# Optimization experiments

Hardware: AMD Instinct MI355X
Metric: run time of the kernel (lower is better)

Reference implementation:

```python
import jax, jax.numpy as jnp
import numpy as np
from jax import lax

INPUT_DIM = 1024
HIDDEN_DIM = 2048
N, L = 64, 512


def setup_inputs() -> dict:
    key = jax.random.key(0)
    ks = jax.random.split(key, 6)
    X = jax.random.normal(ks[0], (N, L, INPUT_DIM), dtype=jnp.float32)
    H0 = jnp.zeros((N, HIDDEN_DIM), dtype=jnp.float32)
    # G-invariant layer params (DeepSets invariant map): out = w * sum(x) + b, one per gate (i,f,g,o)
    inv_scale = 1.0 / np.sqrt(INPUT_DIM)
    inv_w = jax.random.normal(ks[1], (4, HIDDEN_DIM), dtype=jnp.float32) * inv_scale
    inv_b = jax.random.normal(ks[2], (4, HIDDEN_DIM), dtype=jnp.float32) * inv_scale
    # Linear(hidden, hidden) per gate, torch convention W: (out, in)
    lin_scale = 1.0 / np.sqrt(HIDDEN_DIM)
    lin_W = jax.random.normal(ks[3], (4, HIDDEN_DIM, HIDDEN_DIM), dtype=jnp.float32) * lin_scale
    lin_b = jax.random.normal(ks[4], (4, HIDDEN_DIM), dtype=jnp.float32) * lin_scale
    return {"X": X, "H0": H0, "inv_w": inv_w, "inv_b": inv_b, "lin_W": lin_W, "lin_b": lin_b}


def reference(X, H0, inv_w, inv_b, lin_W, lin_b):
    # X: (N, L, D); H0: (N, H)
    def step(carry, x_t):
        h, c = carry                               # (N, H), (N, H)
        s = jnp.sum(x_t, axis=-1, keepdims=True)   # (N, 1) invariant statistic
        inv = s * inv_w[:, None, :] + inv_b[:, None, :]            # (4, N, H)
        lin = jnp.einsum('nh,gkh->gnk', h, lin_W) + lin_b[:, None, :]  # (4, N, H)
        z = inv + lin
        i = jax.nn.sigmoid(z[0])
        f = jax.nn.sigmoid(z[1])
        g = jnp.tanh(z[2])
        o = jax.nn.sigmoid(z[3])
        c = f * c + i * g
        h = o * jnp.tanh(c)
        return (h, c), None

    Xt = jnp.swapaxes(X, 0, 1)                     # (L, N, D)
    (h, _), _ = lax.scan(step, (H0, jnp.zeros_like(H0)), Xt)
    # original returns swapdims(hidden_state, 0, 1) -> (H, N)
    return h.T
```

## Files before the change

kernel.cpp:

```cpp
#include <hip/hip_runtime.h>
#include <hip/hip_fp16.h>


typedef _Float16 f16x8 __attribute__((ext_vector_type(8)));
typedef float    f32x4 __attribute__((ext_vector_type(4)));
typedef unsigned long long u64;

static __device__ __forceinline__ float fast_sig(float x) {
  return 1.f / (1.f + __expf(-x));
}
static __device__ __forceinline__ float fast_tanh(float x) {
  x = fminf(15.f, fmaxf(-15.f, x));
  const float e = __expf(2.f * x);
  return (e - 1.f) / (e + 1.f);
}

static __device__ __forceinline__ void st_h16(void* p, float v) {
  const unsigned short b = __builtin_bit_cast(unsigned short, (_Float16)v);
  __hip_atomic_store((unsigned short*)p, b, __ATOMIC_RELAXED, __HIP_MEMORY_SCOPE_AGENT);
}
static __device__ __forceinline__ void st_h32(void* p, unsigned v) {
  __hip_atomic_store((unsigned*)p, v, __ATOMIC_RELAXED, __HIP_MEMORY_SCOPE_AGENT);
}

static __device__ __forceinline__ int h_off(int n, int j) {
  return ((n >> 4) << 16) + ((j >> 5) << 10) + ((n & 15) << 6) +
         (((j >> 3) & 3) << 4) + ((j & 7) << 1);
}

__global__ void __launch_bounds__(256) seq_sum_kernel(const float* __restrict__ X,
                                                      float* s_all) {
  const int gw   = (int)((blockIdx.x * blockDim.x + threadIdx.x) >> 6);
  const int lane = threadIdx.x & 63;
  const int n = gw >> 9, t = gw & 511;
  const float4* p = (const float4*)(X + ((size_t)gw << 10));
  float s = 0.f;
#pragma unroll
  for (int i = 0; i < 4; ++i) {
    const float4 v = p[lane + (i << 6)];
    s += (v.x + v.y) + (v.z + v.w);
  }
#pragma unroll
  for (int off = 32; off; off >>= 1) s += __shfl_xor(s, off);
  if (lane == 0) s_all[(t << 6) + n] = s;
}

__global__ void bar_init_kernel(unsigned* bar) {
  bar[threadIdx.x]       = 0u;
  bar[threadIdx.x + 256] = 0u;
  bar[threadIdx.x + 512] = 0u;
  bar[threadIdx.x + 768] = 0u;
}

static __device__ __forceinline__ void grid_barrier(unsigned* bar, unsigned round,
                                                    int tid, int blk) {
  asm volatile("s_waitcnt vmcnt(0)" ::: "memory");
  __syncthreads();
  if (tid == 0) {
    __hip_atomic_fetch_add(bar + ((blk & 7) << 4), 1u, __ATOMIC_RELAXED,
                           __HIP_MEMORY_SCOPE_AGENT);
    const unsigned target = round << 8;
    unsigned guard = 0;
    for (;;) {
      unsigned s = 0;
#pragma unroll
      for (int i = 0; i < 8; ++i)
        s += __hip_atomic_load(bar + (i << 4), __ATOMIC_RELAXED,
                               __HIP_MEMORY_SCOPE_AGENT);
      if (s >= target) break;
      __builtin_amdgcn_s_sleep(1);
      if (++guard > (1u << 23)) break;
    }
  }
  __syncthreads();
}

#define LOAD4(d0, d1, d2, d3, addr)                                         \
  asm volatile("global_load_dwordx4 %0, %4, off sc1\n\t"                    \
               "global_load_dwordx4 %1, %4, off offset:1024 sc1\n\t"        \
               "global_load_dwordx4 %2, %4, off offset:2048 sc1\n\t"        \
               "global_load_dwordx4 %3, %4, off offset:3072 sc1"            \
               : "=&v"(d0), "=&v"(d1), "=&v"(d2), "=&v"(d3)                 \
               : "v"(addr)                                                  \
               : "memory")

#define WAITG(n, A)                                                         \
  asm volatile("s_waitcnt vmcnt(" #n ")"                                    \
               : "+v"(A[0]), "+v"(A[1]), "+v"(A[2]), "+v"(A[3]),            \
                 "+v"(A[4]), "+v"(A[5]), "+v"(A[6]), "+v"(A[7]),            \
                 "+v"(A[8]), "+v"(A[9]), "+v"(A[10]), "+v"(A[11]),          \
                 "+v"(A[12]), "+v"(A[13]), "+v"(A[14]), "+v"(A[15])         \
               :                                                            \
               : "memory")

#define KMATH(A)                                                            \
  _Pragma("unroll")                                                         \
  for (int i_ = 0; i_ < 16; ++i_) {                                         \
    acc[0] = __builtin_amdgcn_mfma_f32_16x16x32_f16(A[i_], Wr[i_][0],       \
                                                    acc[0], 0, 0, 0);       \
    acc[1] = __builtin_amdgcn_mfma_f32_16x16x32_f16(A[i_], Wr[i_][1],       \
                                                    acc[1], 0, 0, 0);       \
    acc[2] = __builtin_amdgcn_mfma_f32_16x16x32_f16(A[i_], Wr[i_][2],       \
                                                    acc[2], 0, 0, 0);       \
    acc[3] = __builtin_amdgcn_mfma_f32_16x16x32_f16(A[i_], Wr[i_][3],       \
                                                    acc[3], 0, 0, 0);       \
  }

#define SCATTER(bt)                                                         \
  _Pragma("unroll")                                                         \
  for (int ct_ = 0; ct_ < 4; ++ct_) {                                       \
    const int kf_ = ct_ * 4 + (cc >> 2);                                    \
    _Pragma("unroll")                                                       \
    for (int v_ = 0; v_ < 4; ++v_) {                                        \
      const int n_  = (bt) * 16 + (q << 2) + v_;                            \
      const int key = (n_ & 15) ^ (n_ >> 4);                                \
      red[wave][n_][((kf_ ^ key) << 2) + (cc & 3)] = acc[ct_][v_];          \
    }                                                                       \
  }

__global__ void __launch_bounds__(256, 1) ginv_lstm_persist(
    const float* __restrict__ lin_W, const float* __restrict__ inv_w,
    const float* __restrict__ inv_b, const float* __restrict__ lin_b,
    const float* s_all, const float* __restrict__ H0,
    _Float16* hb0, _Float16* hb1, unsigned* bar, float* out) {
  __shared__ __align__(16) float s_lds[512][32];
  __shared__ __align__(16) float red[4][32][64];
  const int blk = blockIdx.x;
  const int tid = threadIdx.x;
  _Float16* hbuf[2] = {hb0, hb1};

  const int fblk = blk & 127;
  const int nh   = blk >> 7;

  const int wave = tid >> 6;
  const int lane = tid & 63;
  const int q    = lane >> 4;
  const int cc   = lane & 15;

  f16x8 Wr[16][4];
#pragma unroll
  for (int ct = 0; ct < 4; ++ct) {
    const int kf = ct * 4 + (cc >> 2), g = cc & 3;
    const float* wrow =
        lin_W + (((size_t)(g * 2048 + fblk * 16 + kf)) << 11) + wave * 512 + q * 8;
#pragma unroll
    for (int kc = 0; kc < 16; ++kc) {
      const float4 va = *(const float4*)(wrow + kc * 32);
      const float4 vb = *(const float4*)(wrow + kc * 32 + 4);
      f16x8 f;
      f[0] = (_Float16)va.x; f[1] = (_Float16)va.y;
      f[2] = (_Float16)va.z; f[3] = (_Float16)va.w;
      f[4] = (_Float16)vb.x; f[5] = (_Float16)vb.y;
      f[6] = (_Float16)vb.z; f[7] = (_Float16)vb.w;
      Wr[kc][ct] = f;
    }
  }

  {
    int i0 = blk * 512 + tid;
    st_h16((char*)hb0 + h_off(i0 >> 11, i0 & 2047), H0[i0]);
    i0 += 256;
    st_h16((char*)hb0 + h_off(i0 >> 11, i0 & 2047), H0[i0]);
  }

  for (int i = tid; i < 512 * 8; i += 256) {
    const int t4 = i >> 3, nl4 = (i & 7) << 2;
    *(float4*)&s_lds[t4][nl4] =
        *(const float4*)&s_all[(t4 << 6) + (nh << 5) + nl4];
  }

  const int nloc = (wave << 3) + (lane >> 3);
  const int c0   = (lane & 7) << 1;
  float iw[2][4], ibb[2][4];
#pragma unroll
  for (int kk = 0; kk < 2; ++kk) {
    const int Kg = fblk * 16 + c0 + kk;
#pragma unroll
    for (int g = 0; g < 4; ++g) {
      iw[kk][g]  = inv_w[(g << 11) + Kg];
      ibb[kk][g] = inv_b[(g << 11) + Kg] + lin_b[(g << 11) + Kg];
    }
  }

  unsigned round = 1;
  grid_barrier(bar, round, tid, blk);

  float cst[2] = {0.f, 0.f};
  float hnew[2] = {0.f, 0.f};

  const int ld_base = ((nh * 2) << 16) + (wave << 14) + (cc << 6) + (q << 4);
  const int hst_off = ((nh * 2 + (nloc >> 4)) << 16) + ((fblk >> 1) << 10) +
                      ((nloc & 15) << 6) + ((fblk & 1) << 5) + (c0 << 1);
  const int key = (nloc & 15) ^ (nloc >> 4);

  for (int t = 0; t < 512; ++t) {
    const char* hpb = (const char*)hbuf[t & 1] + ld_base;

    f16x8 pa[16], pb[16];
    f32x4 acc[4];

#pragma unroll
    for (int w = 0; w < 4; ++w)
      LOAD4(pa[w * 4], pa[w * 4 + 1], pa[w * 4 + 2], pa[w * 4 + 3],
            hpb + (w << 12));
#pragma unroll
    for (int w = 0; w < 4; ++w)
      LOAD4(pb[w * 4], pb[w * 4 + 1], pb[w * 4 + 2], pb[w * 4 + 3],
            hpb + 65536 + (w << 12));

    WAITG(16, pa);
#pragma unroll
    for (int ct = 0; ct < 4; ++ct) acc[ct] = (f32x4){0.f, 0.f, 0.f, 0.f};
    KMATH(pa);
    SCATTER(0);

    WAITG(0, pb);
#pragma unroll
    for (int ct = 0; ct < 4; ++ct) acc[ct] = (f32x4){0.f, 0.f, 0.f, 0.f};
    KMATH(pb);
    SCATTER(1);

    __syncthreads();

    const float sv = s_lds[t][nloc];
#pragma unroll
    for (int kk = 0; kk < 2; ++kk) {
      const int off = ((c0 + kk) ^ key) << 2;
      f32x4 zz = *(const f32x4*)&red[0][nloc][off];
#pragma unroll
      for (int w = 1; w < 4; ++w) zz += *(const f32x4*)&red[w][nloc][off];
      const float zi = zz[0] + sv * iw[kk][0] + ibb[kk][0];
      const float zf = zz[1] + sv * iw[kk][1] + ibb[kk][1];
      const float zg = zz[2] + sv * iw[kk][2] + ibb[kk][2];
      const float zo = zz[3] + sv * iw[kk][3] + ibb[kk][3];
      const float ig = fast_sig(zi);
      const float fg = fast_sig(zf);
      const float gg = fast_tanh(zg);
      const float og = fast_sig(zo);
      const float cn = fg * cst[kk] + ig * gg;
      cst[kk] = cn;
      hnew[kk] = og * fast_tanh(cn);
    }

    {
      const unsigned lo = __builtin_bit_cast(unsigned short, (_Float16)hnew[0]);
      const unsigned hi = __builtin_bit_cast(unsigned short, (_Float16)hnew[1]);
      st_h32((char*)hbuf[(t + 1) & 1] + hst_off, lo | (hi << 16));
    }
    ++round;
    grid_barrier(bar, round, tid, blk);
  }

#pragma unroll
  for (int kk = 0; kk < 2; ++kk)
    out[((fblk * 16 + c0 + kk) << 6) + (nh << 5) + nloc] = hnew[kk];
}

extern "C" void kernel_launch(void* const* d_in, const int* in_sizes, int n_in,
                              void* d_out, int out_size, void* d_ws, size_t ws_size,
                              hipStream_t stream) {
  const float* X     = (const float*)d_in[0];
  const float* H0    = (const float*)d_in[1];
  const float* inv_w = (const float*)d_in[2];
  const float* inv_b = (const float*)d_in[3];
  const float* lin_W = (const float*)d_in[4];
  const float* lin_b = (const float*)d_in[5];
  float* out = (float*)d_out;

  const size_t S_BYTES = 512 * 64 * 4;
  const size_t BAR_PAD = 4096;
  const size_t H_BYTES = 64 * 2048 * 2;
  const size_t NEED = S_BYTES + BAR_PAD + 2 * H_BYTES;

  float*    s_all;
  unsigned* bar;
  _Float16* hb[2];
  if (ws_size >= NEED) {
    char* ws = (char*)d_ws;
    s_all = (float*)ws;
    bar   = (unsigned*)(ws + S_BYTES);
    for (int i = 0; i < 2; ++i)
      hb[i] = (_Float16*)(ws + S_BYTES + BAR_PAD + (size_t)i * H_BYTES);
  } else {
    s_all = (float*)d_out;
    char* xt = (char*)d_in[0] + (size_t)64 * 512 * 1024 * 4 -
               (BAR_PAD + 2 * H_BYTES);
    bar = (unsigned*)xt;
    for (int i = 0; i < 2; ++i)
      hb[i] = (_Float16*)(xt + BAR_PAD + (size_t)i * H_BYTES);
  }

  seq_sum_kernel<<<8192, 256, 0, stream>>>(X, s_all);
  bar_init_kernel<<<1, 256, 0, stream>>>(bar);
  ginv_lstm_persist<<<256, 256, 0, stream>>>(lin_W, inv_w, inv_b, lin_b, s_all, H0,
                                             hb[0], hb[1], bar, out);
}
```

Baseline: 4.194 ms.

## Use two-level tree grid barrier and staggered per-chunk load waits

Replaces the flat grid barrier, where each waiting block polled eight counters, with a hierarchy. Blocks increment a group counter, the last arrival in each group bumps a root counter, and waiters spin on that single root word. Separately, the single wait on all sixteen loads of each half is split into four waits on four-load chunks, so MFMA work starts as soon as each chunk arrives. This cuts polling traffic and overlaps load latency with compute, but lengthens the barrier's critical path by one extra atomic and depends on the block-to-group mapping and counter layout being correct.

```diff
diff --git a/kernel.cpp b/kernel.cpp
--- a/kernel.cpp
+++ b/kernel.cpp
@@ -57,17 +57,17 @@
   asm volatile("s_waitcnt vmcnt(0)" ::: "memory");
   __syncthreads();
   if (tid == 0) {
-    __hip_atomic_fetch_add(bar + ((blk & 7) << 4), 1u, __ATOMIC_RELAXED,
-                           __HIP_MEMORY_SCOPE_AGENT);
-    const unsigned target = round << 8;
+    unsigned* base = bar + ((blk >> 7) << 8);
+    unsigned* grp  = base + ((blk & 3) << 4);
+    unsigned* root = base + 128;
+    const unsigned old =
+        __hip_atomic_fetch_add(grp, 1u, __ATOMIC_RELAXED, __HIP_MEMORY_SCOPE_AGENT);
+    if (old == 32u * round - 1u)
+      __hip_atomic_fetch_add(root, 1u, __ATOMIC_RELAXED, __HIP_MEMORY_SCOPE_AGENT);
+    const unsigned target = round << 2;
     unsigned guard = 0;
-    for (;;) {
-      unsigned s = 0;
-#pragma unroll
-      for (int i = 0; i < 8; ++i)
-        s += __hip_atomic_load(bar + (i << 4), __ATOMIC_RELAXED,
-                               __HIP_MEMORY_SCOPE_AGENT);
-      if (s >= target) break;
+    while (__hip_atomic_load(root, __ATOMIC_RELAXED, __HIP_MEMORY_SCOPE_AGENT) <
+           target) {
       __builtin_amdgcn_s_sleep(1);
       if (++guard > (1u << 23)) break;
     }
@@ -84,18 +84,16 @@
                : "v"(addr)                                                  \
                : "memory")
 
-#define WAITG(n, A)                                                         \
+#define WAITG4(n, A, b)                                                     \
   asm volatile("s_waitcnt vmcnt(" #n ")"                                    \
-               : "+v"(A[0]), "+v"(A[1]), "+v"(A[2]), "+v"(A[3]),            \
-                 "+v"(A[4]), "+v"(A[5]), "+v"(A[6]), "+v"(A[7]),            \
-                 "+v"(A[8]), "+v"(A[9]), "+v"(A[10]), "+v"(A[11]),          \
-                 "+v"(A[12]), "+v"(A[13]), "+v"(A[14]), "+v"(A[15])         \
+               : "+v"(A[(b)]), "+v"(A[(b) + 1]), "+v"(A[(b) + 2]),          \
+                 "+v"(A[(b) + 3])                                           \
                :                                                            \
                : "memory")
 
-#define KMATH(A)                                                            \
+#define KMATH4(A, b)                                                        \
   _Pragma("unroll")                                                         \
-  for (int i_ = 0; i_ < 16; ++i_) {                                         \
+  for (int i_ = (b); i_ < (b) + 4; ++i_) {                                  \
     acc[0] = __builtin_amdgcn_mfma_f32_16x16x32_f16(A[i_], Wr[i_][0],       \
                                                     acc[0], 0, 0, 0);       \
     acc[1] = __builtin_amdgcn_mfma_f32_16x16x32_f16(A[i_], Wr[i_][1],       \
@@ -208,16 +206,20 @@
       LOAD4(pb[w * 4], pb[w * 4 + 1], pb[w * 4 + 2], pb[w * 4 + 3],
             hpb + 65536 + (w << 12));
 
-    WAITG(16, pa);
 #pragma unroll
     for (int ct = 0; ct < 4; ++ct) acc[ct] = (f32x4){0.f, 0.f, 0.f, 0.f};
-    KMATH(pa);
+    WAITG4(28, pa, 0);  KMATH4(pa, 0);
+    WAITG4(24, pa, 4);  KMATH4(pa, 4);
+    WAITG4(20, pa, 8);  KMATH4(pa, 8);
+    WAITG4(16, pa, 12); KMATH4(pa, 12);
     SCATTER(0);
 
-    WAITG(0, pb);
 #pragma unroll
     for (int ct = 0; ct < 4; ++ct) acc[ct] = (f32x4){0.f, 0.f, 0.f, 0.f};
-    KMATH(pb);
+    WAITG4(12, pb, 0);  KMATH4(pb, 0);
+    WAITG4(8,  pb, 4);  KMATH4(pb, 4);
+    WAITG4(4,  pb, 8);  KMATH4(pb, 8);
+    WAITG4(0,  pb, 12); KMATH4(pb, 12);
     SCATTER(1);
 
     __syncthreads();
```

After: 3.897 ms. 1.08x faster.
